# Kernel optimization log

Measured on AMD Instinct MI355X. Metric: run time of the kernel, lower is better.

Reference implementation:

```python
import jax, jax.numpy as jnp
from jax import lax
import numpy as np

K_RAW, S_RAW, P_RAW = 4, 2, 1
K_CORR, S_CORR, P_CORR, D_CORR = 3, 1, 1, 1
FUSE_K = 3
SOFTMAX_SCALE = 10.0
NEG_BIG = -1e9  # stands in for -inf added to masked patches (softmax -> ~0)


def _patches(img, k, s, p, d=1):
    # (n,c,h,w) -> (n, c*k*k, ho, wo); channel ordering (c, kh, kw) matches torch.nn.functional.unfold
    return lax.conv_general_dilated_patches(img, (k, k), (s, s), [(p, p), (p, p)], rhs_dilation=(d, d))


def _conv_eye(m, kern):
    # 2D conv with the 'eye' fuse kernel, stride 1, same padding
    pad = (FUSE_K - 1) // 2
    return lax.conv_general_dilated(m, kern, (1, 1), [(pad, pad), (pad, pad)],
                                    dimension_numbers=('NCHW', 'OIHW', 'NCHW'))


def _deconv(score, filt, k, s, p):
    # torch conv_transpose2d for one sample: score (L,h,w), filt (L,c,k,k) -> (c, H, W)
    rhs = jnp.flip(filt.transpose(1, 0, 2, 3), (2, 3))  # (c, L, k, k), spatially flipped
    pad = k - 1 - p
    out = lax.conv_general_dilated(score[None], rhs, (1, 1), [(pad, pad), (pad, pad)],
                                   lhs_dilation=(s, s),
                                   dimension_numbers=('NCHW', 'OIHW', 'NCHW'))
    return out[0]


def _forward(x, context, mask):
    n, c, h, w = x.shape
    # --- raw context patches (patch-copy filters), torch unfold order ---
    raw_p = _patches(context, K_RAW, S_RAW, P_RAW)           # (n, c*16, hr, wr)
    hr, wr = raw_p.shape[2], raw_p.shape[3]
    Lr = hr * wr
    raw_filter = raw_p.reshape(n, c * K_RAW * K_RAW, Lr).transpose(0, 2, 1)
    raw_filter = raw_filter.reshape(n, Lr, c, K_RAW, K_RAW)
    xs = x[:, :, ::2, ::2]
    cs = context[:, :, ::2, ::2]
    # --- L2-normalized context patches for correlation ---
    cp = _patches(cs, K_CORR, S_CORR, P_CORR, D_CORR)        # (n, c*9, hu, wu)
    hu, wu = cp.shape[2], cp.shape[3]
    L = hu * wu
    cols = cp.reshape(n, c * K_CORR * K_CORR, L).transpose(0, 2, 1)  # (n, L, c*9)
    norm = jnp.sqrt(jnp.sum(cols * cols, axis=2, keepdims=True))
    cols = cols / jnp.maximum(norm, jnp.asarray(1e-4, cols.dtype))
    # --- patch correlation: grouped conv == einsum over unfolded x ---
    xp = _patches(xs, K_CORR, S_CORR, P_CORR, D_CORR)        # (n, c*9, hm, wm)
    hm, wm = xp.shape[2], xp.shape[3]
    corr = jnp.einsum('nkhw,nlk->nlhw', xp, cols)            # (n, L, hm, wm)
    # --- fuse correlation map with eye kernels (literal translation) ---
    eye = jnp.eye(FUSE_K, dtype=corr.dtype).reshape(1, 1, FUSE_K, FUSE_K)
    m_ = corr.transpose(0, 2, 3, 1).reshape(n, 1, hm * wm, hu * wu)
    m_ = _conv_eye(m_, eye)
    m_ = m_.reshape(n, hu, wu, hm, wm).transpose(0, 2, 1, 4, 3).reshape(n, 1, hu * wu, hm * wm)
    m_ = _conv_eye(m_, eye)
    corr = m_.reshape(n, wu, hu, wm, hm).transpose(0, 4, 3, 2, 1).reshape(n, -1, hu, wu)
    # --- mask: any masked pixel in a patch => patch excluded from softmax ---
    ms = mask[:, :, ::2, ::2]
    mp = _patches(ms, K_CORR, S_CORR, P_CORR, D_CORR)        # (n, 9, hu, wu)
    masked = (jnp.sum(mp, axis=1) > 0).reshape(n, L, 1, 1)
    corr = corr + jnp.where(masked, jnp.asarray(NEG_BIG, corr.dtype), jnp.asarray(0.0, corr.dtype))
    # --- softmax over patch dim ---
    att = jax.nn.softmax(corr * SOFTMAX_SCALE, axis=1)       # (n, L, hu, wu)
    # --- weighted patch copy via per-sample conv_transpose ---
    out = jax.vmap(lambda a, f: _deconv(a, f, K_RAW, S_RAW, P_RAW))(att, raw_filter)  # (n, c, h, w)
    # --- overlap normalization ---
    ones_in = jnp.ones((1, hu, wu), att.dtype)
    ones_f = jnp.ones((1, 1, K_RAW, K_RAW), att.dtype)
    overlap = _deconv(ones_in, ones_f, K_RAW, S_RAW, P_RAW)  # (1, h, w)
    overlap = jnp.where(overlap == 0, jnp.asarray(1.0, att.dtype), overlap)
    out = out / overlap[None]
    att_score = att.reshape(n, hu, wu, hu, wu)
    return out, att_score


def setup_inputs() -> dict:
    key = jax.random.key(0)
    k1, k2 = jax.random.split(key)
    N, C, H, W = 4, 96, 96, 96
    x = jax.random.normal(k1, (N, C, H, W), jnp.float32)
    context = jax.random.normal(k2, (N, C, H, W), jnp.float32)
    # rectangular inpainting hole (1 = masked), as in DeepFill training
    mask = jnp.zeros((N, 1, H, W), jnp.float32).at[:, :, 32:64, 32:64].set(1.0)
    return {"x": x, "context": context, "mask": mask}


def reference(x, context, mask):
    return _forward(x, context, mask)
```

## Files before the change

### kernel.cpp

```cpp
#include <hip/hip_runtime.h>
#include <stdint.h>

#define BN_ 4
#define CC 96
#define HF 96
#define WF 96
#define HS 48
#define WS 48
#define LL 2304
#define J2 1536
#define NEG10 (-1.0e10f)
#define NLB 72

typedef __attribute__((ext_vector_type(8))) _Float16 half8v;
typedef __attribute__((ext_vector_type(4))) float float4v;
typedef float float4u __attribute__((ext_vector_type(4), aligned(4)));

__device__ __forceinline__ int Tswap(int f) { return (f % 48) * 48 + f / 48; }

__device__ __forceinline__ unsigned short f2h(float f) {
    _Float16 h = (_Float16)f;
    return __builtin_bit_cast(unsigned short, h);
}
__device__ __forceinline__ float h2f(unsigned short u) {
    return (float)__builtin_bit_cast(_Float16, u);
}

typedef const __attribute__((address_space(1))) uint32_t* gas_ptr;
typedef __attribute__((address_space(3))) uint32_t* las_ptr;
__device__ __forceinline__ void gload16(const void* g, void* l) {
    __builtin_amdgcn_global_load_lds((gas_ptr)g, (las_ptr)l, 16, 0, 0);
}

__global__ void ssum_kernel(const float* __restrict__ ctx, float* __restrict__ ssum) {
    int idx = blockIdx.x * 256 + threadIdx.x;
    if (idx >= BN_ * HS * WS) return;
    int j = idx % WS, i = (idx / WS) % HS, n = idx / (WS * HS);
    float s = 0.f;
    for (int c = 0; c < CC; ++c) {
        float v = ctx[((size_t)(n * CC + c) * HF + 2 * i) * WF + 2 * j];
        s += v * v;
    }
    ssum[idx] = s;
}

__global__ void invn_kernel(const float* __restrict__ ssum, float* __restrict__ invn) {
    int idx = blockIdx.x * 256 + threadIdx.x;
    if (idx >= BN_ * LL) return;
    int l = idx % LL, n = idx / LL;
    int i0 = l / WS, j0 = l % WS;
    float s = 0.f;
    for (int dy = -1; dy <= 1; ++dy)
        for (int dx = -1; dx <= 1; ++dx) {
            int i = i0 + dy, j = j0 + dx;
            if (i >= 0 && i < HS && j >= 0 && j < WS)
                s += ssum[(n * HS + i) * WS + j];
        }
    invn[idx] = 1.f / fmaxf(sqrtf(s), 1e-4f);
}

__global__ void mask_kernel(const float* __restrict__ mask, float* __restrict__ maskadd) {
    int idx = blockIdx.x * 256 + threadIdx.x;
    if (idx >= BN_ * LL) return;
    int l = idx % LL, n = idx / LL;
    int i0 = l / WS, j0 = l % WS;
    float s = 0.f;
    for (int dy = -1; dy <= 1; ++dy)
        for (int dx = -1; dx <= 1; ++dx) {
            int i = i0 + dy, j = j0 + dx;
            if (i >= 0 && i < HS && j >= 0 && j < WS)
                s += mask[(size_t)n * HF * WF + (2 * i) * WF + 2 * j];
        }
    maskadd[idx] = (s > 0.f) ? NEG10 : 0.f;
}

__global__ void slice_split2(const float* __restrict__ ctx, const float* __restrict__ x,
                             unsigned short* __restrict__ cs_hi, unsigned short* __restrict__ cs_lo,
                             unsigned short* __restrict__ xs_hi, unsigned short* __restrict__ xs_lo) {
    int idx = blockIdx.x * 256 + threadIdx.x;
    if (idx >= BN_ * LL * CC) return;
    const float* src = blockIdx.y ? x : ctx;
    unsigned short* hi = blockIdx.y ? xs_hi : cs_hi;
    unsigned short* lo = blockIdx.y ? xs_lo : cs_lo;
    int c = idx % CC;
    int u = (idx / CC) % LL;
    int n = idx / (CC * LL);
    int i = u / WS, j = u % WS;
    float v = src[((size_t)(n * CC + c) * HF + 2 * i) * WF + 2 * j];
    unsigned short h = f2h(v);
    hi[idx] = h;
    lo[idx] = f2h(v - h2f(h));
}

__global__ void rf_split(const float* __restrict__ ctx, unsigned short* __restrict__ hf) {
    int idx = blockIdx.x * 256 + threadIdx.x;
    if (idx >= BN_ * J2 * LL) return;
    int l = idx % LL;
    int j = (idx / LL) % J2;
    int n = idx / (LL * J2);
    int c = j >> 4, ky = (j >> 2) & 3, kx = j & 3;
    int y = 2 * (l / WS) + ky - 1;
    int x = 2 * (l % WS) + kx - 1;
    float v = 0.f;
    if (y >= 0 && y < HF && x >= 0 && x < WF)
        v = ctx[((size_t)(n * CC + c) * HF + y) * WF + x];
    hf[idx] = f2h(v);
}

__global__ __launch_bounds__(256, 4) void gemm_split3(
    const unsigned short* __restrict__ Ah_, const unsigned short* __restrict__ Al_,
    const unsigned short* __restrict__ Bh_, const unsigned short* __restrict__ Bl_,
    float* __restrict__ Cout, int M_, int N_, int K_, int nbx, int nby)
{
    __shared__ unsigned short lds[4][128][32];

    int wg = blockIdx.x;
    int wgid = (wg & 7) * (gridDim.x >> 3) + (wg >> 3);
    int bx = wgid % nbx;
    int t1 = wgid / nbx;
    int by = t1 % nby;
    int bz = t1 / nby;
    const int m0 = by * 128, n0 = bx * 128;
    const int t = threadIdx.x;

    const size_t sA = (size_t)M_ * K_, sB = (size_t)N_ * K_;
    const unsigned short* Ah = Ah_ + (size_t)bz * sA;
    const unsigned short* Al = Al_ + (size_t)bz * sA;
    const unsigned short* Bh = Bh_ + (size_t)bz * sB;
    const unsigned short* Bl = Bl_ + (size_t)bz * sB;

    const int rloc = t >> 2;
    const int sst = t & 3;
    const int kg = sst ^ ((rloc >> 1) & 3);
    const size_t offA0 = (size_t)(m0 + rloc) * K_ + kg * 8;
    const size_t offA1 = (size_t)(m0 + 64 + rloc) * K_ + kg * 8;
    const size_t offB0 = (size_t)(n0 + rloc) * K_ + kg * 8;
    const size_t offB1 = (size_t)(n0 + 64 + rloc) * K_ + kg * 8;
    const unsigned short* gp0 = Ah + offA0;
    const unsigned short* gp1 = Ah + offA1;
    const unsigned short* gp2 = Al + offA0;
    const unsigned short* gp3 = Al + offA1;
    const unsigned short* gp4 = Bh + offB0;
    const unsigned short* gp5 = Bh + offB1;
    const unsigned short* gp6 = Bl + offB0;
    const unsigned short* gp7 = Bl + offB1;
    unsigned short* lp0 = &lds[0][rloc][sst * 8];
    unsigned short* lp1 = &lds[0][64 + rloc][sst * 8];
    unsigned short* lp2 = &lds[1][rloc][sst * 8];
    unsigned short* lp3 = &lds[1][64 + rloc][sst * 8];
    unsigned short* lp4 = &lds[2][rloc][sst * 8];
    unsigned short* lp5 = &lds[2][64 + rloc][sst * 8];
    unsigned short* lp6 = &lds[3][rloc][sst * 8];
    unsigned short* lp7 = &lds[3][64 + rloc][sst * 8];

    const int lane = t & 63;
    const int w = t >> 6, wr = w >> 1, wc = w & 1;
    const int lr = lane & 15, lg = lane >> 4;

    float4v acc[4][4] = {};
    const int nt = K_ / 32;

    for (int kt = 0; kt < nt; ++kt) {
        __syncthreads();
        gload16(gp0, lp0); gload16(gp1, lp1);
        gload16(gp2, lp2); gload16(gp3, lp3);
        gload16(gp4, lp4); gload16(gp5, lp5);
        gload16(gp6, lp6); gload16(gp7, lp7);
        gp0 += 32; gp1 += 32; gp2 += 32; gp3 += 32;
        gp4 += 32; gp5 += 32; gp6 += 32; gp7 += 32;
        __syncthreads();

        half8v bh[4], bl[4];
#pragma unroll
        for (int j = 0; j < 4; ++j) {
            int row = wc * 64 + j * 16 + lr;
            int s = (lg ^ ((row >> 1) & 3)) * 8;
            bh[j] = *(const half8v*)&lds[2][row][s];
            bl[j] = *(const half8v*)&lds[3][row][s];
        }
#pragma unroll
        for (int i = 0; i < 4; ++i) {
            int row = wr * 64 + i * 16 + lr;
            int s = (lg ^ ((row >> 1) & 3)) * 8;
            half8v ah = *(const half8v*)&lds[0][row][s];
            half8v al = *(const half8v*)&lds[1][row][s];
#pragma unroll
            for (int j = 0; j < 4; ++j) {
                acc[i][j] = __builtin_amdgcn_mfma_f32_16x16x32_f16(ah, bh[j], acc[i][j], 0, 0, 0);
                acc[i][j] = __builtin_amdgcn_mfma_f32_16x16x32_f16(ah, bl[j], acc[i][j], 0, 0, 0);
                acc[i][j] = __builtin_amdgcn_mfma_f32_16x16x32_f16(al, bh[j], acc[i][j], 0, 0, 0);
            }
        }
    }

    float* Cb = Cout + (size_t)bz * M_ * N_;
#pragma unroll
    for (int i = 0; i < 4; ++i) {
        int mb = m0 + wr * 64 + i * 16 + lg * 4;
#pragma unroll
        for (int j = 0; j < 4; ++j) {
            int nn = n0 + wc * 64 + j * 16 + lr;
#pragma unroll
            for (int r = 0; r < 4; ++r)
                Cb[(size_t)(mb + r) * N_ + nn] = acc[i][j][r];
        }
    }
}

__global__ __launch_bounds__(256, 4) void gemm_k64(
    const unsigned short* __restrict__ Ah_, const unsigned short* __restrict__ Bh_,
    unsigned short* __restrict__ Cout, int M_, int N_, int K_, int nbx, int nby)
{
    __shared__ unsigned short lds[2][128][64];

    int wg = blockIdx.x;
    int wgid = (wg & 7) * (gridDim.x >> 3) + (wg >> 3);
    int bx = wgid % nbx;
    int t1 = wgid / nbx;
    int by = t1 % nby;
    int bz = t1 / nby;
    const int m0 = by * 128, n0 = bx * 128;
    const int t = threadIdx.x;

    const unsigned short* Ah = Ah_ + (size_t)bz * M_ * K_;
    const unsigned short* Bh = Bh_ + (size_t)bz * N_ * K_;

    const unsigned short* gpA[4];
    const unsigned short* gpB[4];
    int lo[4];
#pragma unroll
    for (int rep = 0; rep < 4; ++rep) {
        int slot = t + rep * 256;
        int row = slot >> 3, sc = slot & 7;
        int kg = sc ^ (row & 7);
        gpA[rep] = Ah + (size_t)(m0 + row) * K_ + kg * 8;
        gpB[rep] = Bh + (size_t)(n0 + row) * K_ + kg * 8;
        lo[rep] = row * 64 + sc * 8;
    }

    const int lane = t & 63;
    const int w = t >> 6, wr = w >> 1, wc = w & 1;
    const int lr = lane & 15, lg = lane >> 4;

    float4v acc[4][4] = {};
    const int nt = K_ / 64;
    unsigned short* LA = &lds[0][0][0];
    unsigned short* LB = &lds[1][0][0];

    for (int kt = 0; kt < nt; ++kt) {
        __syncthreads();
#pragma unroll
        for (int rep = 0; rep < 4; ++rep) {
            gload16(gpA[rep], LA + lo[rep]);
            gload16(gpB[rep], LB + lo[rep]);
            gpA[rep] += 64; gpB[rep] += 64;
        }
        __syncthreads();
#pragma unroll
        for (int kk = 0; kk < 2; ++kk) {
            half8v bh[4];
#pragma unroll
            for (int j = 0; j < 4; ++j) {
                int row = wc * 64 + j * 16 + lr;
                int sc = (kk * 4 + lg) ^ (row & 7);
                bh[j] = *(const half8v*)&lds[1][row][sc * 8];
            }
#pragma unroll
            for (int i = 0; i < 4; ++i) {
                int row = wr * 64 + i * 16 + lr;
                int sc = (kk * 4 + lg) ^ (row & 7);
                half8v ah = *(const half8v*)&lds[0][row][sc * 8];
#pragma unroll
                for (int j = 0; j < 4; ++j)
                    acc[i][j] = __builtin_amdgcn_mfma_f32_16x16x32_f16(ah, bh[j], acc[i][j], 0, 0, 0);
            }
        }
    }

    unsigned short* Gb = Cout + (size_t)bz * M_ * N_;
#pragma unroll
    for (int i = 0; i < 4; ++i) {
        int mb = m0 + wr * 64 + i * 16 + lg * 4;
#pragma unroll
        for (int j = 0; j < 4; ++j) {
            int nn = n0 + wc * 64 + j * 16 + lr;
#pragma unroll
            for (int r = 0; r < 4; ++r)
                Gb[(size_t)(mb + r) * N_ + nn] = f2h(acc[i][j][r]);
        }
    }
}

__global__ void gatherS(const float* __restrict__ E, const float* __restrict__ invn,
                        float* __restrict__ S) {
    int wg = blockIdx.x;
    int wgid = (wg & 7) * (gridDim.x >> 3) + (wg >> 3);
    int idx = wgid * 256 + threadIdx.x;
    int q = idx % 576;
    int l = (idx / 576) % LL;
    int n = idx / (576 * LL);
    int p0 = q * 4;
    int li = l / WS, lj = l % WS;
    int pi = p0 / WS, pj = p0 % WS;
    const float* Eb = E + (size_t)n * LL * LL;
    float4v acc = {0.f, 0.f, 0.f, 0.f};
#pragma unroll
    for (int dy = -1; dy <= 1; ++dy) {
        if (li + dy < 0 || li + dy >= HS) continue;
        if (pi + dy < 0 || pi + dy >= HS) continue;
#pragma unroll
        for (int dx = -1; dx <= 1; ++dx) {
            if (lj + dx < 0 || lj + dx >= WS) continue;
            int k = dy * WS + dx;
            const float* row = &Eb[(size_t)(l + k) * LL];
            float4u v = *(const float4u*)&row[p0 + k];
            bool v0 = (pj + dx >= 0);
            bool v3 = (pj + 3 + dx < WS);
            if (v0) acc[0] += v[0];
            acc[1] += v[1];
            acc[2] += v[2];
            if (v3) acc[3] += v[3];
        }
    }
    float iv = invn[n * LL + l];
    float4v outv;
#pragma unroll
    for (int i = 0; i < 4; ++i) outv[i] = acc[i] * iv;
    *(float4v*)&S[((size_t)n * LL + l) * LL + p0] = outv;
}

__global__ __launch_bounds__(256) void fuse_stat(const float* __restrict__ S,
                                                 const float* __restrict__ maskadd,
                                                 float* __restrict__ F,
                                                 float* __restrict__ pm,
                                                 float* __restrict__ ps) {
    __shared__ float msh[4][256], ssh[4][256];
    int wg = blockIdx.x;
    int wgid = (wg & 7) * (gridDim.x >> 3) + (wg >> 3);
    int pb = wgid % 9;
    int t1 = wgid / 9;
    int lb = t1 % NLB;
    int n = t1 / NLB;
    int tq = threadIdx.x & 63, tl = threadIdx.x >> 6;
    int p0 = pb * 256 + tq * 4;
    const float* Sb = S + (size_t)n * LL * LL;
    const float* mb = maskadd + n * LL;
    float* Fb = F + (size_t)n * LL * LL;

    int Tp0 = Tswap(p0);
    int p2b[3]; bool pok[3], v0m[3], v1m[3], v2m[3], v3m[3];
#pragma unroll
    for (int d = 0; d < 3; ++d) {
        int fp0 = Tp0 + d - 1;
        pok[d] = (fp0 < LL);
        int ee = (fp0 < 0) ? 1 : 0;
        p2b[d] = Tswap(fp0 + 48 * ee) - ee;
        v0m[d] = (fp0 >= 0);
        v1m[d] = (fp0 + 48 < LL);
        v2m[d] = (fp0 + 96 < LL);
        v3m[d] = (fp0 + 144 < LL);
    }

    float mreg[4] = {-3e38f, -3e38f, -3e38f, -3e38f};
    float sreg[4] = {0.f, 0.f, 0.f, 0.f};

    for (int it = 0; it < 8; ++it) {
        int l = lb * 32 + it * 4 + tl;
        int Tl = Tswap(l);
        float4v acc = {0.f, 0.f, 0.f, 0.f};
#pragma unroll
        for (int d = 0; d < 3; ++d) {
            int fl = Tl + d - 1;
            if (fl < 0 || fl >= LL || !pok[d]) continue;
            int l2 = Tswap(fl);
#pragma unroll
            for (int d1 = -1; d1 <= 1; ++d1) {
                int l3 = l2 + d1;
                if (l3 < 0 || l3 >= LL) continue;
                int pc = p2b[d] + d1;
                float4u v = *(const float4u*)&Sb[(size_t)l3 * LL + pc];
                if (v0m[d] && pc >= 0 && pc < LL)          acc[0] += v[0];
                if (v1m[d] && pc + 1 >= 0 && pc + 1 < LL)  acc[1] += v[1];
                if (v2m[d] && pc + 2 < LL)                 acc[2] += v[2];
                if (v3m[d] && pc + 3 < LL)                 acc[3] += v[3];
            }
        }
        float madd = mb[l];
        float4v f;
#pragma unroll
        for (int i = 0; i < 4; ++i) {
            f[i] = acc[i] * 10.f + madd;
            float mm = fmaxf(mreg[i], f[i]);
            sreg[i] = sreg[i] * __expf(mreg[i] - mm) + __expf(f[i] - mm);
            mreg[i] = mm;
        }
        *(float4v*)&Fb[(size_t)l * LL + p0] = f;
    }

#pragma unroll
    for (int i = 0; i < 4; ++i) { msh[tl][tq * 4 + i] = mreg[i]; ssh[tl][tq * 4 + i] = sreg[i]; }
    __syncthreads();
    if (tl == 0) {
#pragma unroll
        for (int i = 0; i < 4; ++i) {
            float m = msh[0][tq * 4 + i], s = ssh[0][tq * 4 + i];
#pragma unroll
            for (int r = 1; r < 4; ++r) {
                float m2 = msh[r][tq * 4 + i], s2 = ssh[r][tq * 4 + i];
                float mm = fmaxf(m, m2);
                s = s * __expf(m - mm) + s2 * __expf(m2 - mm);
                m = mm;
            }
            pm[((size_t)n * NLB + lb) * LL + p0 + i] = m;
            ps[((size_t)n * NLB + lb) * LL + p0 + i] = s;
        }
    }
}

__global__ void mergestat_kernel(const float* __restrict__ pm, const float* __restrict__ ps,
                                 float* __restrict__ mstat, float* __restrict__ sinv) {
    int idx = blockIdx.x * 256 + threadIdx.x;
    if (idx >= BN_ * LL) return;
    int n = idx / LL, p = idx % LL;
    float m = -3e38f, s = 0.f;
    for (int q = 0; q < NLB; ++q) {
        float m2 = pm[((size_t)n * NLB + q) * LL + p];
        float s2 = ps[((size_t)n * NLB + q) * LL + p];
        float mm = fmaxf(m, m2);
        s = s * __expf(m - mm) + s2 * __expf(m2 - mm);
        m = mm;
    }
    mstat[idx] = m;
    sinv[idx] = 1.f / s;
}

__global__ __launch_bounds__(256) void finish_kernel(const float* __restrict__ F,
                                                     const float* __restrict__ mstat,
                                                     const float* __restrict__ sinv,
                                                     float* __restrict__ att,
                                                     unsigned short* __restrict__ Th) {
    __shared__ float tile[64][65];
    int n = blockIdx.z;
    int l0 = blockIdx.y * 64, p0 = blockIdx.x * 64;
    const float* Fb = F + (size_t)n * LL * LL;
    float* Ab = att + (size_t)n * LL * LL;
    int tx = threadIdx.x & 15, ty = threadIdx.x >> 4;
    float4v m4 = *(const float4v*)&mstat[n * LL + p0 + tx * 4];
    float4v s4 = *(const float4v*)&sinv[n * LL + p0 + tx * 4];
#pragma unroll
    for (int q = 0; q < 4; ++q) {
        int lr = q * 16 + ty;
        float4v v = *(const float4v*)&Fb[(size_t)(l0 + lr) * LL + p0 + tx * 4];
        float4v e;
#pragma unroll
        for (int i = 0; i < 4; ++i) e[i] = __expf(v[i] - m4[i]) * s4[i];
        *(float4v*)&Ab[(size_t)(l0 + lr) * LL + p0 + tx * 4] = e;
#pragma unroll
        for (int i = 0; i < 4; ++i) tile[lr][tx * 4 + i] = e[i];
    }
    __syncthreads();
    int pr = threadIdx.x >> 2, lq = threadIdx.x & 3;
    uint32_t u[8];
#pragma unroll
    for (int i = 0; i < 8; ++i) {
        unsigned short h0 = f2h(tile[lq * 16 + 2 * i][pr]);
        unsigned short h1 = f2h(tile[lq * 16 + 2 * i + 1][pr]);
        u[i] = (uint32_t)h0 | ((uint32_t)h1 << 16);
    }
    unsigned short* dst = &Th[((size_t)n * LL + p0 + pr) * LL + l0 + lq * 16];
    ((uint32_t*)dst)[0] = u[0]; ((uint32_t*)dst)[1] = u[1];
    ((uint32_t*)dst)[2] = u[2]; ((uint32_t*)dst)[3] = u[3];
    ((uint32_t*)dst)[4] = u[4]; ((uint32_t*)dst)[5] = u[5];
    ((uint32_t*)dst)[6] = u[6]; ((uint32_t*)dst)[7] = u[7];
}

__global__ void col2im_kernel(const unsigned short* __restrict__ G, float* __restrict__ out) {
    int idx = blockIdx.x * 256 + threadIdx.x;
    if (idx >= BN_ * CC * HF * WF) return;
    int x = idx % WF;
    int y = (idx / WF) % HF;
    int c = (idx / (WF * HF)) % CC;
    int n = idx / (WF * HF * CC);
    const unsigned short* Gb = G + (size_t)n * LL * J2;
    float acc = 0.f;
#pragma unroll
    for (int ky = 0; ky < 4; ++ky) {
        int ynum = y + 1 - ky;
        if (ynum & 1) continue;
        int iy = ynum >> 1;
        if (iy < 0 || iy >= HS) continue;
#pragma unroll
        for (int kx = 0; kx < 4; ++kx) {
            int xnum = x + 1 - kx;
            if (xnum & 1) continue;
            int ix = xnum >> 1;
            if (ix < 0 || ix >= WS) continue;
            acc += h2f(Gb[(size_t)(iy * WS + ix) * J2 + c * 16 + ky * 4 + kx]);
        }
    }
    float cy = (y == 0 || y == HF - 1) ? 1.f : 2.f;
    float cx = (x == 0 || x == WF - 1) ? 1.f : 2.f;
    out[idx] = acc / (cy * cx);
}

extern "C" void kernel_launch(void* const* d_in, const int* in_sizes, int n_in,
                              void* d_out, int out_size, void* d_ws, size_t ws_size,
                              hipStream_t stream) {
    const float* x       = (const float*)d_in[0];
    const float* context = (const float*)d_in[1];
    const float* mask    = (const float*)d_in[2];

    float* out = (float*)d_out;
    float* att_region = out + (size_t)BN_ * CC * HF * WF;

    char* wsb = (char*)d_ws;
    const size_t ESL = (size_t)BN_ * LL * CC;
    const size_t ERF = (size_t)BN_ * J2 * LL;
    unsigned short* Th = (unsigned short*)wsb;
    float* pm    = (float*)(wsb + 42467328);
    float* ps    = (float*)(wsb + 45121536);
    float* mstat = (float*)(wsb + 47775744);
    float* sinv  = (float*)(wsb + 47812608);
    float* invn  = (float*)(wsb + 47849472);
    float* ssum  = (float*)(wsb + 47886336);
    unsigned short* cs_hi = (unsigned short*)(wsb + 47923200);
    unsigned short* cs_lo = cs_hi + ESL;
    unsigned short* xs_hi = cs_lo + ESL;
    unsigned short* xs_lo = xs_hi + ESL;
    float* E = (float*)(wsb + 63700992);
    float* F = (float*)(wsb + 63700992);
    unsigned short* RF = (unsigned short*)(wsb + 63700992);
    unsigned short* G  = (unsigned short*)(wsb + 92012544);
    float* maskadd = (float*)(wsb + 148635648);
    float* S = att_region;

    ssum_kernel<<<(BN_ * HS * WS + 255) / 256, 256, 0, stream>>>(context, ssum);
    invn_kernel<<<(BN_ * LL + 255) / 256, 256, 0, stream>>>(ssum, invn);
    mask_kernel<<<(BN_ * LL + 255) / 256, 256, 0, stream>>>(mask, maskadd);

    slice_split2<<<dim3((int)(ESL / 256), 2), 256, 0, stream>>>(
        context, x, cs_hi, cs_lo, xs_hi, xs_lo);

    gemm_split3<<<(LL / 128) * (LL / 128) * BN_, 256, 0, stream>>>(
        cs_hi, cs_lo, xs_hi, xs_lo, E, LL, LL, CC, LL / 128, LL / 128);

    gatherS<<<(int)((size_t)BN_ * LL * 576 / 256), 256, 0, stream>>>(E, invn, S);

    fuse_stat<<<9 * NLB * BN_, 256, 0, stream>>>(S, maskadd, F, pm, ps);
    mergestat_kernel<<<(BN_ * LL + 255) / 256, 256, 0, stream>>>(pm, ps, mstat, sinv);
    finish_kernel<<<dim3(LL / 64, LL / 64, BN_), 256, 0, stream>>>(F, mstat, sinv, att_region, Th);

    rf_split<<<(int)(ERF / 256), 256, 0, stream>>>(context, RF);

    gemm_k64<<<(J2 / 128) * (LL / 128) * BN_, 256, 0, stream>>>(
        Th, RF, G, LL, J2, LL, J2 / 128, LL / 128);

    col2im_kernel<<<(BN_ * CC * HF * WF + 255) / 256, 256, 0, stream>>>(G, out);
}
```

Measured before the change: 356.1 us.

## Recompute fused scores in finish kernel instead of storing F; merge invn/mask kernels

Stops fuse_stat from writing the full fused-score matrix F to memory. Instead, finish_fuse recomputes the 9-tap fuse sum from S while applying the softmax normalisation. To make room, buffers are swapped: the GEMM output E now lives in the att output region and S sits in the workspace. The invn and mask kernels are also merged into one launch. This saves a large write and read of F at the cost of repeating the gather arithmetic, which means nine reads of S per output element in the finish pass.

```diff
diff --git a/kernel.cpp b/kernel.cpp
--- a/kernel.cpp
+++ b/kernel.cpp
@@ -44,34 +44,23 @@
     ssum[idx] = s;
 }
 
-__global__ void invn_kernel(const float* __restrict__ ssum, float* __restrict__ invn) {
+__global__ void invnmask_kernel(const float* __restrict__ ssum, const float* __restrict__ mask,
+                                float* __restrict__ invn, float* __restrict__ maskadd) {
     int idx = blockIdx.x * 256 + threadIdx.x;
     if (idx >= BN_ * LL) return;
     int l = idx % LL, n = idx / LL;
     int i0 = l / WS, j0 = l % WS;
-    float s = 0.f;
+    float s = 0.f, ms = 0.f;
     for (int dy = -1; dy <= 1; ++dy)
         for (int dx = -1; dx <= 1; ++dx) {
             int i = i0 + dy, j = j0 + dx;
-            if (i >= 0 && i < HS && j >= 0 && j < WS)
+            if (i >= 0 && i < HS && j >= 0 && j < WS) {
                 s += ssum[(n * HS + i) * WS + j];
+                ms += mask[(size_t)n * HF * WF + (2 * i) * WF + 2 * j];
+            }
         }
     invn[idx] = 1.f / fmaxf(sqrtf(s), 1e-4f);
-}
-
-__global__ void mask_kernel(const float* __restrict__ mask, float* __restrict__ maskadd) {
-    int idx = blockIdx.x * 256 + threadIdx.x;
-    if (idx >= BN_ * LL) return;
-    int l = idx % LL, n = idx / LL;
-    int i0 = l / WS, j0 = l % WS;
-    float s = 0.f;
-    for (int dy = -1; dy <= 1; ++dy)
-        for (int dx = -1; dx <= 1; ++dx) {
-            int i = i0 + dy, j = j0 + dx;
-            if (i >= 0 && i < HS && j >= 0 && j < WS)
-                s += mask[(size_t)n * HF * WF + (2 * i) * WF + 2 * j];
-        }
-    maskadd[idx] = (s > 0.f) ? NEG10 : 0.f;
+    maskadd[idx] = (ms > 0.f) ? NEG10 : 0.f;
 }
 
 __global__ void slice_split2(const float* __restrict__ ctx, const float* __restrict__ x,
@@ -331,7 +320,6 @@
 
 __global__ __launch_bounds__(256) void fuse_stat(const float* __restrict__ S,
                                                  const float* __restrict__ maskadd,
-                                                 float* __restrict__ F,
                                                  float* __restrict__ pm,
                                                  float* __restrict__ ps) {
     __shared__ float msh[4][256], ssh[4][256];
@@ -345,7 +333,6 @@
     int p0 = pb * 256 + tq * 4;
     const float* Sb = S + (size_t)n * LL * LL;
     const float* mb = maskadd + n * LL;
-    float* Fb = F + (size_t)n * LL * LL;
 
     int Tp0 = Tswap(p0);
     int p2b[3]; bool pok[3], v0m[3], v1m[3], v2m[3], v3m[3];
@@ -374,10 +361,10 @@
             if (fl < 0 || fl >= LL || !pok[d]) continue;
             int l2 = Tswap(fl);
 #pragma unroll
-            for (int d1 = -1; d1 <= 1; ++d1) {
-                int l3 = l2 + d1;
+            for (int d1 = 0; d1 < 3; ++d1) {
+                int l3 = l2 + d1 - 1;
                 if (l3 < 0 || l3 >= LL) continue;
-                int pc = p2b[d] + d1;
+                int pc = p2b[d] + d1 - 1;
                 float4u v = *(const float4u*)&Sb[(size_t)l3 * LL + pc];
                 if (v0m[d] && pc >= 0 && pc < LL)          acc[0] += v[0];
                 if (v1m[d] && pc + 1 >= 0 && pc + 1 < LL)  acc[1] += v[1];
@@ -386,15 +373,13 @@
             }
         }
         float madd = mb[l];
-        float4v f;
 #pragma unroll
         for (int i = 0; i < 4; ++i) {
-            f[i] = acc[i] * 10.f + madd;
-            float mm = fmaxf(mreg[i], f[i]);
-            sreg[i] = sreg[i] * __expf(mreg[i] - mm) + __expf(f[i] - mm);
+            float f = acc[i] * 10.f + madd;
+            float mm = fmaxf(mreg[i], f);
+            sreg[i] = sreg[i] * __expf(mreg[i] - mm) + __expf(f - mm);
             mreg[i] = mm;
         }
-        *(float4v*)&Fb[(size_t)l * LL + p0] = f;
     }
 
 #pragma unroll
@@ -434,27 +419,68 @@
     sinv[idx] = 1.f / s;
 }
 
-__global__ __launch_bounds__(256) void finish_kernel(const float* __restrict__ F,
-                                                     const float* __restrict__ mstat,
-                                                     const float* __restrict__ sinv,
-                                                     float* __restrict__ att,
-                                                     unsigned short* __restrict__ Th) {
+__global__ __launch_bounds__(256) void finish_fuse(const float* __restrict__ S,
+                                                   const float* __restrict__ maskadd,
+                                                   const float* __restrict__ mstat,
+                                                   const float* __restrict__ sinv,
+                                                   float* __restrict__ att,
+                                                   unsigned short* __restrict__ Th) {
     __shared__ float tile[64][65];
     int n = blockIdx.z;
     int l0 = blockIdx.y * 64, p0 = blockIdx.x * 64;
-    const float* Fb = F + (size_t)n * LL * LL;
+    const float* Sb = S + (size_t)n * LL * LL;
+    const float* mb = maskadd + n * LL;
     float* Ab = att + (size_t)n * LL * LL;
     int tx = threadIdx.x & 15, ty = threadIdx.x >> 4;
-    float4v m4 = *(const float4v*)&mstat[n * LL + p0 + tx * 4];
-    float4v s4 = *(const float4v*)&sinv[n * LL + p0 + tx * 4];
+    int pq = p0 + tx * 4;
+    float4v m4 = *(const float4v*)&mstat[n * LL + pq];
+    float4v s4 = *(const float4v*)&sinv[n * LL + pq];
+
+    int Tp0 = Tswap(pq);
+    int p2b[3]; bool pok[3], v0m[3], v1m[3], v2m[3], v3m[3];
+#pragma unroll
+    for (int d = 0; d < 3; ++d) {
+        int fp0 = Tp0 + d - 1;
+        pok[d] = (fp0 < LL);
+        int ee = (fp0 < 0) ? 1 : 0;
+        p2b[d] = Tswap(fp0 + 48 * ee) - ee;
+        v0m[d] = (fp0 >= 0);
+        v1m[d] = (fp0 + 48 < LL);
+        v2m[d] = (fp0 + 96 < LL);
+        v3m[d] = (fp0 + 144 < LL);
+    }
+
 #pragma unroll
     for (int q = 0; q < 4; ++q) {
         int lr = q * 16 + ty;
-        float4v v = *(const float4v*)&Fb[(size_t)(l0 + lr) * LL + p0 + tx * 4];
+        int l = l0 + lr;
+        int Tl = Tswap(l);
+        float4v acc = {0.f, 0.f, 0.f, 0.f};
+#pragma unroll
+        for (int d = 0; d < 3; ++d) {
+            int fl = Tl + d - 1;
+            if (fl < 0 || fl >= LL || !pok[d]) continue;
+            int l2 = Tswap(fl);
+#pragma unroll
+            for (int d1 = 0; d1 < 3; ++d1) {
+                int l3 = l2 + d1 - 1;
+                if (l3 < 0 || l3 >= LL) continue;
+                int pc = p2b[d] + d1 - 1;
+                float4u v = *(const float4u*)&Sb[(size_t)l3 * LL + pc];
+                if (v0m[d] && pc >= 0 && pc < LL)          acc[0] += v[0];
+                if (v1m[d] && pc + 1 >= 0 && pc + 1 < LL)  acc[1] += v[1];
+                if (v2m[d] && pc + 2 < LL)                 acc[2] += v[2];
+                if (v3m[d] && pc + 3 < LL)                 acc[3] += v[3];
+            }
+        }
+        float madd = mb[l];
         float4v e;
 #pragma unroll
-        for (int i = 0; i < 4; ++i) e[i] = __expf(v[i] - m4[i]) * s4[i];
-        *(float4v*)&Ab[(size_t)(l0 + lr) * LL + p0 + tx * 4] = e;
+        for (int i = 0; i < 4; ++i) {
+            float F = acc[i] * 10.f + madd;
+            e[i] = __expf(F - m4[i]) * s4[i];
+        }
+        *(float4v*)&Ab[(size_t)l * LL + pq] = e;
 #pragma unroll
         for (int i = 0; i < 4; ++i) tile[lr][tx * 4 + i] = e[i];
     }
@@ -527,16 +553,14 @@
     unsigned short* cs_lo = cs_hi + ESL;
     unsigned short* xs_hi = cs_lo + ESL;
     unsigned short* xs_lo = xs_hi + ESL;
-    float* E = (float*)(wsb + 63700992);
-    float* F = (float*)(wsb + 63700992);
+    float* S = (float*)(wsb + 63700992);
     unsigned short* RF = (unsigned short*)(wsb + 63700992);
     unsigned short* G  = (unsigned short*)(wsb + 92012544);
     float* maskadd = (float*)(wsb + 148635648);
-    float* S = att_region;
+    float* E = att_region;
 
     ssum_kernel<<<(BN_ * HS * WS + 255) / 256, 256, 0, stream>>>(context, ssum);
-    invn_kernel<<<(BN_ * LL + 255) / 256, 256, 0, stream>>>(ssum, invn);
-    mask_kernel<<<(BN_ * LL + 255) / 256, 256, 0, stream>>>(mask, maskadd);
+    invnmask_kernel<<<(BN_ * LL + 255) / 256, 256, 0, stream>>>(ssum, mask, invn, maskadd);
 
     slice_split2<<<dim3((int)(ESL / 256), 2), 256, 0, stream>>>(
         context, x, cs_hi, cs_lo, xs_hi, xs_lo);
@@ -546,9 +570,11 @@
 
     gatherS<<<(int)((size_t)BN_ * LL * 576 / 256), 256, 0, stream>>>(E, invn, S);
 
-    fuse_stat<<<9 * NLB * BN_, 256, 0, stream>>>(S, maskadd, F, pm, ps);
+    fuse_stat<<<9 * NLB * BN_, 256, 0, stream>>>(S, maskadd, pm, ps);
     mergestat_kernel<<<(BN_ * LL + 255) / 256, 256, 0, stream>>>(pm, ps, mstat, sinv);
-    finish_kernel<<<dim3(LL / 64, LL / 64, BN_), 256, 0, stream>>>(F, mstat, sinv, att_region, Th);
+
+    finish_fuse<<<dim3(LL / 64, LL / 64, BN_), 256, 0, stream>>>(
+        S, maskadd, mstat, sinv, att_region, Th);
 
     rf_split<<<(int)(ERF / 256), 256, 0, stream>>>(context, RF);
 
```

Result: slower. 401.1 us (+12.6%).
